# Performance work log

Measured on AMD Instinct MI355X. Metric: run time of the kernel, lower is better.

## Reference

```python
import jax, jax.numpy as jnp
import numpy as np

N_NODES = 100000
N_EDGES = 1600000


def setup_inputs() -> dict:
    key = jax.random.key(0)
    ks = jax.random.split(key, 8)
    x = jax.random.normal(ks[0], (N_NODES, 100), dtype=jnp.float32)
    edge_index = jax.random.randint(ks[1], (2, N_EDGES), 0, N_NODES, dtype=jnp.int64)
    edge_weight = jax.random.uniform(ks[2], (N_EDGES,), dtype=jnp.float32)
    # params (kaiming-ish scale)
    W_conv = jax.random.normal(ks[3], (100, 32), dtype=jnp.float32) * (1.0 / np.sqrt(100))
    b_conv = jnp.zeros((32,), jnp.float32)
    W1 = jax.random.normal(ks[4], (32, 16), dtype=jnp.float32) * (1.0 / np.sqrt(32))
    b1 = jnp.zeros((16,), jnp.float32)
    W2 = jax.random.normal(ks[5], (16, 8), dtype=jnp.float32) * (1.0 / np.sqrt(16))
    b2 = jnp.zeros((8,), jnp.float32)
    W3 = jax.random.normal(ks[6], (8, 10), dtype=jnp.float32) * (1.0 / np.sqrt(8))
    b3 = jnp.zeros((10,), jnp.float32)
    return {"x": x, "edge_index": edge_index, "edge_weight": edge_weight,
            "W_conv": W_conv, "b_conv": b_conv, "W1": W1, "b1": b1,
            "W2": W2, "b2": b2, "W3": W3, "b3": b3}


def gcn_conv(x, edge_index, W, b, n_nodes):
    # PyG GCNConv: add self-loops, symmetric deg^-0.5 normalization, unit edge weights
    loop = jnp.arange(n_nodes, dtype=edge_index.dtype)
    src = jnp.concatenate([edge_index[0], loop])
    dst = jnp.concatenate([edge_index[1], loop])
    deg = jax.ops.segment_sum(jnp.ones_like(dst, dtype=x.dtype), dst,
                              num_segments=n_nodes)
    dinv = jax.lax.rsqrt(jnp.maximum(deg, 1e-12))  # deg >= 1 due to self-loops
    norm = dinv[src] * dinv[dst]                   # [E+N]
    h = x @ W                                      # [N, 32]
    msg = h[src] * norm[:, None]                   # gather + scale
    out = jax.ops.segment_sum(msg, dst, num_segments=n_nodes)  # scatter-add
    return out + b


def reference(x, edge_index, edge_weight, W_conv, b_conv, W1, b1, W2, b2, W3, b3):
    # edge_weight is accepted by the original forward but never used (conv1(x, edge_index))
    n_nodes = x.shape[0]
    h = jax.nn.relu(gcn_conv(x, edge_index, W_conv, b_conv, n_nodes))
    # F.dropout with training=False (eval) is identity
    h = jax.nn.relu(h @ W1 + b1)
    h = jax.nn.relu(h @ W2 + b2)
    h = h @ W3 + b3
    return jax.nn.log_softmax(h, axis=1)
```

## Files before the change

kernel.cpp:

```cpp
#include <hip/hip_runtime.h>
#include <hip/hip_fp16.h>
#include <math.h>

#define N_NODES 100000
#define N_EDGES 1600000
#define F_IN 100
#define F_H 32

#define BKT_SHIFT 7
#define BKT_C 128
#define NBK 782
#define BKT_CAP 2560

#define BF_B 1024
#define BF_EPT 8
#define BF_TILE 8192
#define BF_GRID 196

#define XW_ROWS 256
#define XW_S2 51
#define XW_GRID 391

#define FUSE_GRID (BF_GRID + XW_GRID)
#define SM_BYTES 58624

#define AG_B 512
#define AG_CAP BKT_CAP
#define AG_EPT 5

__global__ __launch_bounds__(BF_B) void fused1_kernel(
        const int* __restrict__ src, const int* __restrict__ dst,
        int* __restrict__ gcursor, unsigned* __restrict__ packed,
        const float* __restrict__ x, const float* __restrict__ W,
        float* __restrict__ h2f) {
    __shared__ char smraw[SM_BYTES] __attribute__((aligned(16)));
    int t = threadIdx.x;
    if (blockIdx.x < BF_GRID) {
        int* cnt = (int*)smraw;
        int* lbase = cnt + NBK;
        int* gbase = lbase + NBK;
        int* wsums = gbase + NBK;
        int* ptot = wsums + 16;
        unsigned* stage = (unsigned*)(ptot + 1);
        unsigned short* stageB = (unsigned short*)(stage + BF_TILE);
        long base = (long)blockIdx.x * BF_TILE;
        for (int i = t; i < NBK; i += BF_B) cnt[i] = 0;
        __syncthreads();
        int myb[BF_EPT]; int mypos[BF_EPT]; unsigned mypk[BF_EPT];
#pragma unroll
        for (int k = 0; k < BF_EPT; k++) {
            long e = base + t + (long)k * BF_B;
            myb[k] = -1;
            if (e < N_EDGES) {
                int d = dst[e];
                int sI = src[e];
                int b = d >> BKT_SHIFT;
                myb[k] = b;
                mypk[k] = (unsigned)sI | ((unsigned)(d & (BKT_C - 1)) << 17);
                mypos[k] = atomicAdd(&cnt[b], 1);
            }
        }
        __syncthreads();
        if (t < NBK && cnt[t] > 0)
            gbase[t] = t * BKT_CAP + atomicAdd(&gcursor[t], cnt[t]);
        int lane = t & 63, w = t >> 6;
        int v = (t < NBK) ? cnt[t] : 0;
        int sc = v;
#pragma unroll
        for (int off = 1; off < 64; off <<= 1) {
            int xx = __shfl_up(sc, off, 64);
            if (lane >= off) sc += xx;
        }
        if (lane == 63) wsums[w] = sc;
        __syncthreads();
        int pre = 0;
#pragma unroll
        for (int u = 0; u < 16; u++) pre += (u < w) ? wsums[u] : 0;
        int incl = sc + pre;
        if (t < NBK) lbase[t] = incl - v;
        if (t == BF_B - 1) ptot[0] = incl;
        __syncthreads();
#pragma unroll
        for (int k = 0; k < BF_EPT; k++) {
            if (myb[k] >= 0) {
                int p = lbase[myb[k]] + mypos[k];
                stage[p] = mypk[k];
                stageB[p] = (unsigned short)myb[k];
            }
        }
        __syncthreads();
        int T = ptot[0];
        for (int i = t; i < T; i += BF_B) {
            int b = stageB[i];
            packed[gbase[b] + (i - lbase[b])] = stage[i];
        }
    } else {
        __half2* xs = (__half2*)smraw;
        int rbase = (blockIdx.x - BF_GRID) * XW_ROWS;
        int rows = min(XW_ROWS, N_NODES - rbase);
        int total = rows * F_IN;
        const float4* gx4 = (const float4*)(x + (long)rbase * F_IN);
        for (int i4 = t; i4 < (total >> 2); i4 += BF_B) {
            float4 v = gx4[i4];
            int i = i4 << 2;
            int r = i / F_IN;
            int k = i - r * F_IN;
            __half2* p = xs + r * XW_S2 + (k >> 1);
            p[0] = __floats2half2_rn(v.x, v.y);
            p[1] = __floats2half2_rn(v.z, v.w);
        }
        __syncthreads();
        int r = t & (XW_ROWS - 1);
        int colbase = __builtin_amdgcn_readfirstlane((t >> 8) << 3);
        if (r < rows) {
            const float* Wp = W + colbase;
            float acc[8];
#pragma unroll
            for (int j = 0; j < 8; j++) acc[j] = 0.f;
            const __half2* xr = xs + r * XW_S2;
#pragma unroll 5
            for (int k2 = 0; k2 < F_IN / 2; k2++) {
                float2 xv = __half22float2(xr[k2]);
#pragma unroll
                for (int j = 0; j < 8; j++)
                    acc[j] = fmaf(xv.y, Wp[(2 * k2 + 1) * F_H + j],
                                  fmaf(xv.x, Wp[(2 * k2) * F_H + j], acc[j]));
            }
            float4* dst4 = (float4*)(h2f + (long)(rbase + r) * F_H + colbase);
            dst4[0] = make_float4(acc[0], acc[1], acc[2], acc[3]);
            dst4[1] = make_float4(acc[4], acc[5], acc[6], acc[7]);
        }
    }
}

__global__ __launch_bounds__(256) void scale_kernel(
        const int* __restrict__ blen, const unsigned* __restrict__ packed,
        const float* __restrict__ h2f, __half* __restrict__ h2) {
    __shared__ int cnt[BKT_C];
    __shared__ float sdv[BKT_C];
    int t = threadIdx.x;
    int b = blockIdx.x;
    if (t < BKT_C) cnt[t] = 0;
    __syncthreads();
    int beg = b * BKT_CAP, end = beg + blen[b];
    for (int i = beg + t; i < end; i += 256)
        atomicAdd(&cnt[(packed[i] >> 17) & (BKT_C - 1)], 1);
    __syncthreads();
    if (t < BKT_C) sdv[t] = rsqrtf((float)cnt[t] + 1.0f);
    __syncthreads();
    int rbase = b << BKT_SHIFT;
    int rows = min(BKT_C, N_NODES - rbase);
    const float4* src4 = (const float4*)(h2f + (long)rbase * F_H);
    float2* dst2 = (float2*)h2;
    for (int i4 = t; i4 < rows * 8; i4 += 256) {
        float4 v = src4[i4];
        float dv = sdv[i4 >> 3];
        float2 o;
        __half2* oh = (__half2*)&o;
        oh[0] = __floats2half2_rn(v.x * dv, v.y * dv);
        oh[1] = __floats2half2_rn(v.z * dv, v.w * dv);
        dst2[(long)rbase * 8 + i4] = o;
    }
}

__global__ __launch_bounds__(AG_B) void agg_kernel(
        const int* __restrict__ blen, const unsigned* __restrict__ packed,
        const __half* __restrict__ h2,
        const float* __restrict__ bc,
        const float* __restrict__ W1, const float* __restrict__ b1,
        const float* __restrict__ W2, const float* __restrict__ b2,
        const float* __restrict__ W3, const float* __restrict__ b3,
        float* __restrict__ out) {
    __shared__ float accL[BKT_C * 33];
    __shared__ int esrc[AG_CAP];
    __shared__ int cnt[BKT_C];
    __shared__ int lbase[BKT_C];
    __shared__ int wsum;
    __shared__ float sbc[32], sW1[512], sb1[16], sW2[128], sb2[8], sW3[80], sb3[10];
    int t = threadIdx.x;
    if (t < 32) sbc[t] = bc[t];
    if (t < 512) sW1[t] = W1[t];
    if (t < 16) sb1[t] = b1[t];
    if (t < 128) sW2[t] = W2[t];
    if (t < 8) sb2[t] = b2[t];
    if (t < 80) sW3[t] = W3[t];
    if (t < 10) sb3[t] = b3[t];

    int b = blockIdx.x;
    int beg = b * BKT_CAP;
    int cnum = blen[b];
    if (t < BKT_C) cnt[t] = 0;
    __syncthreads();
    unsigned pk[AG_EPT]; int pos[AG_EPT];
#pragma unroll
    for (int k = 0; k < AG_EPT; k++) {
        int idx = t + k * AG_B;
        pk[k] = 0xFFFFFFFFu;
        if (idx < cnum) {
            unsigned p = packed[beg + idx];
            pk[k] = p;
            pos[k] = atomicAdd(&cnt[(p >> 17) & (BKT_C - 1)], 1);
        }
    }
    __syncthreads();
    {
        int lane = t & 63;
        int v = 0;
        if (t < BKT_C) {
            v = cnt[t];
#pragma unroll
            for (int off = 1; off < 64; off <<= 1) {
                int xx = __shfl_up(v, off, 64);
                if (lane >= off) v += xx;
            }
            if (t == 63) wsum = v;
        }
        __syncthreads();
        if (t < BKT_C) {
            if (t >= 64) v += wsum;
            lbase[t] = v;
        }
    }
    __syncthreads();
#pragma unroll
    for (int k = 0; k < AG_EPT; k++) {
        if (pk[k] != 0xFFFFFFFFu) {
            int lid = (pk[k] >> 17) & (BKT_C - 1);
            esrc[lbase[lid] - cnt[lid] + pos[k]] = (int)(pk[k] & 0x1FFFF);
        }
    }
    __syncthreads();
    {
        int g = t >> 2, l = t & 3;
        const float4* h2o = (const float4*)h2;
        int e = lbase[g] - cnt[g];
        int eend = lbase[g];
        float a0 = 0.f, a1 = 0.f, a2 = 0.f, a3 = 0.f;
        float a4 = 0.f, a5 = 0.f, a6 = 0.f, a7 = 0.f;
        for (; e + 8 <= eend; e += 8) {
            int s0 = esrc[e], s1 = esrc[e+1], s2 = esrc[e+2], s3 = esrc[e+3];
            int s4 = esrc[e+4], s5 = esrc[e+5], s6 = esrc[e+6], s7 = esrc[e+7];
            float4 q0 = h2o[s0 * 4 + l];
            float4 q1 = h2o[s1 * 4 + l];
            float4 q2 = h2o[s2 * 4 + l];
            float4 q3 = h2o[s3 * 4 + l];
            float4 q4 = h2o[s4 * 4 + l];
            float4 q5 = h2o[s5 * 4 + l];
            float4 q6 = h2o[s6 * 4 + l];
            float4 q7 = h2o[s7 * 4 + l];
#pragma unroll
            for (int u = 0; u < 8; u++) {
                float4 q = (u == 0) ? q0 : (u == 1) ? q1 : (u == 2) ? q2 :
                           (u == 3) ? q3 : (u == 4) ? q4 : (u == 5) ? q5 :
                           (u == 6) ? q6 : q7;
                const __half2* hp = (const __half2*)&q;
                float2 f0 = __half22float2(hp[0]);
                float2 f1 = __half22float2(hp[1]);
                float2 f2 = __half22float2(hp[2]);
                float2 f3 = __half22float2(hp[3]);
                a0 += f0.x; a1 += f0.y; a2 += f1.x; a3 += f1.y;
                a4 += f2.x; a5 += f2.y; a6 += f3.x; a7 += f3.y;
            }
        }
        for (; e < eend; e++) {
            float4 q = h2o[esrc[e] * 4 + l];
            const __half2* hp = (const __half2*)&q;
            float2 f0 = __half22float2(hp[0]);
            float2 f1 = __half22float2(hp[1]);
            float2 f2 = __half22float2(hp[2]);
            float2 f3 = __half22float2(hp[3]);
            a0 += f0.x; a1 += f0.y; a2 += f1.x; a3 += f1.y;
            a4 += f2.x; a5 += f2.y; a6 += f3.x; a7 += f3.y;
        }
        float* ap = accL + g * 33 + 8 * l;
        ap[0] = a0; ap[1] = a1; ap[2] = a2; ap[3] = a3;
        ap[4] = a4; ap[5] = a5; ap[6] = a6; ap[7] = a7;
    }
    __syncthreads();

    int n = (b << BKT_SHIFT) + t;
    if (t < BKT_C && n < N_NODES) {
        float dv = rsqrtf((float)cnt[t] + 1.0f);
        const __half2* h2v = (const __half2*)h2;
        float a[32];
#pragma unroll
        for (int q = 0; q < 16; q++) {
            float2 hv = __half22float2(h2v[n * 16 + q]);
            a[2*q]   = fmaxf((accL[t * 33 + 2*q]   + hv.x) * dv + sbc[2*q],   0.f);
            a[2*q+1] = fmaxf((accL[t * 33 + 2*q+1] + hv.y) * dv + sbc[2*q+1], 0.f);
        }
        float t1[16];
#pragma unroll
        for (int j = 0; j < 16; j++) {
            float s = sb1[j];
            for (int k = 0; k < 32; k++) s += a[k] * sW1[k * 16 + j];
            t1[j] = fmaxf(s, 0.f);
        }
        float t2[8];
#pragma unroll
        for (int j = 0; j < 8; j++) {
            float s = sb2[j];
            for (int k = 0; k < 16; k++) s += t1[k] * sW2[k * 8 + j];
            t2[j] = fmaxf(s, 0.f);
        }
        float t3[10];
#pragma unroll
        for (int j = 0; j < 10; j++) {
            float s = sb3[j];
            for (int k = 0; k < 8; k++) s += t2[k] * sW3[k * 10 + j];
            t3[j] = s;
        }
        float m = t3[0];
#pragma unroll
        for (int j = 1; j < 10; j++) m = fmaxf(m, t3[j]);
        float se = 0.f;
#pragma unroll
        for (int j = 0; j < 10; j++) se += expf(t3[j] - m);
        float lse = logf(se) + m;
        float* op = out + (long)n * 10;
#pragma unroll
        for (int j = 0; j < 10; j++) op[j] = t3[j] - lse;
    }
}

extern "C" void kernel_launch(void* const* d_in, const int* in_sizes, int n_in,
                              void* d_out, int out_size, void* d_ws, size_t ws_size,
                              hipStream_t stream) {
    const float* x  = (const float*)d_in[0];
    const int*   ei = (const int*)d_in[1];
    const float* Wc = (const float*)d_in[3];
    const float* bc = (const float*)d_in[4];
    const float* W1 = (const float*)d_in[5];
    const float* b1 = (const float*)d_in[6];
    const float* W2 = (const float*)d_in[7];
    const float* b2 = (const float*)d_in[8];
    const float* W3 = (const float*)d_in[9];
    const float* b3 = (const float*)d_in[10];
    float* out = (float*)d_out;

    __half*   h2      = (__half*)d_ws;
    unsigned* packed  = (unsigned*)((char*)d_ws + (long)N_NODES * F_H * 2);
    float*    h2f     = (float*)(packed + (long)NBK * BKT_CAP);
    int*      gcursor = (int*)(h2f + (long)N_NODES * F_H);

    const int* srcp = ei;
    const int* dstp = ei + N_EDGES;

    hipMemsetAsync(gcursor, 0, NBK * sizeof(int), stream);
    fused1_kernel<<<FUSE_GRID, BF_B, 0, stream>>>(srcp, dstp, gcursor, packed,
                                                  x, Wc, h2f);
    scale_kernel<<<NBK, 256, 0, stream>>>(gcursor, packed, h2f, h2);
    agg_kernel<<<NBK, AG_B, 0, stream>>>(gcursor, packed, h2, bc, W1, b1,
                                         W2, b2, W3, b3, out);
}
```

Before: 171.0 us.

## Fuse scale and aggregate kernels via cooperative grid sync; halve XW block count

```diff
diff --git a/kernel.cpp b/kernel.cpp
--- a/kernel.cpp
+++ b/kernel.cpp
@@ -1,6 +1,9 @@
 #include <hip/hip_runtime.h>
 #include <hip/hip_fp16.h>
+#include <hip/hip_cooperative_groups.h>
 #include <math.h>
+
+namespace cg = cooperative_groups;
 
 #define N_NODES 100000
 #define N_EDGES 1600000
@@ -19,9 +22,10 @@
 
 #define XW_ROWS 256
 #define XW_S2 51
-#define XW_GRID 391
-
-#define FUSE_GRID (BF_GRID + XW_GRID)
+#define XW_BLOCKS 196
+#define XW_TILES 2
+
+#define FUSE_GRID (BF_GRID + XW_BLOCKS)
 #define SM_BYTES 58624
 
 #define AG_B 512
@@ -96,40 +100,218 @@
         }
     } else {
         __half2* xs = (__half2*)smraw;
-        int rbase = (blockIdx.x - BF_GRID) * XW_ROWS;
-        int rows = min(XW_ROWS, N_NODES - rbase);
-        int total = rows * F_IN;
-        const float4* gx4 = (const float4*)(x + (long)rbase * F_IN);
-        for (int i4 = t; i4 < (total >> 2); i4 += BF_B) {
-            float4 v = gx4[i4];
-            int i = i4 << 2;
-            int r = i / F_IN;
-            int k = i - r * F_IN;
-            __half2* p = xs + r * XW_S2 + (k >> 1);
-            p[0] = __floats2half2_rn(v.x, v.y);
-            p[1] = __floats2half2_rn(v.z, v.w);
-        }
-        __syncthreads();
-        int r = t & (XW_ROWS - 1);
-        int colbase = __builtin_amdgcn_readfirstlane((t >> 8) << 3);
-        if (r < rows) {
-            const float* Wp = W + colbase;
-            float acc[8];
-#pragma unroll
-            for (int j = 0; j < 8; j++) acc[j] = 0.f;
-            const __half2* xr = xs + r * XW_S2;
+        for (int tile = 0; tile < XW_TILES; ++tile) {
+            int tb = (blockIdx.x - BF_GRID) * XW_TILES + tile;
+            int rbase = tb * XW_ROWS;
+            int rows = min(XW_ROWS, N_NODES - rbase);
+            if (rows <= 0) break;
+            if (tile) __syncthreads();
+            int total = rows * F_IN;
+            const float4* gx4 = (const float4*)(x + (long)rbase * F_IN);
+            for (int i4 = t; i4 < (total >> 2); i4 += BF_B) {
+                float4 v = gx4[i4];
+                int i = i4 << 2;
+                int r = i / F_IN;
+                int k = i - r * F_IN;
+                __half2* p = xs + r * XW_S2 + (k >> 1);
+                p[0] = __floats2half2_rn(v.x, v.y);
+                p[1] = __floats2half2_rn(v.z, v.w);
+            }
+            __syncthreads();
+            int r = t & (XW_ROWS - 1);
+            int colbase = __builtin_amdgcn_readfirstlane((t >> 8) << 3);
+            if (r < rows) {
+                const float* Wp = W + colbase;
+                float acc[8];
+#pragma unroll
+                for (int j = 0; j < 8; j++) acc[j] = 0.f;
+                const __half2* xr = xs + r * XW_S2;
 #pragma unroll 5
-            for (int k2 = 0; k2 < F_IN / 2; k2++) {
-                float2 xv = __half22float2(xr[k2]);
-#pragma unroll
-                for (int j = 0; j < 8; j++)
-                    acc[j] = fmaf(xv.y, Wp[(2 * k2 + 1) * F_H + j],
-                                  fmaf(xv.x, Wp[(2 * k2) * F_H + j], acc[j]));
-            }
-            float4* dst4 = (float4*)(h2f + (long)(rbase + r) * F_H + colbase);
-            dst4[0] = make_float4(acc[0], acc[1], acc[2], acc[3]);
-            dst4[1] = make_float4(acc[4], acc[5], acc[6], acc[7]);
-        }
+                for (int k2 = 0; k2 < F_IN / 2; k2++) {
+                    float2 xv = __half22float2(xr[k2]);
+#pragma unroll
+                    for (int j = 0; j < 8; j++)
+                        acc[j] = fmaf(xv.y, Wp[(2 * k2 + 1) * F_H + j],
+                                      fmaf(xv.x, Wp[(2 * k2) * F_H + j], acc[j]));
+                }
+                float4* dst4 = (float4*)(h2f + (long)(rbase + r) * F_H + colbase);
+                dst4[0] = make_float4(acc[0], acc[1], acc[2], acc[3]);
+                dst4[1] = make_float4(acc[4], acc[5], acc[6], acc[7]);
+            }
+        }
+    }
+}
+
+__global__ __launch_bounds__(AG_B, 8) void scagg_kernel(
+        const int* __restrict__ blen, const unsigned* __restrict__ packed,
+        const float* __restrict__ h2f, __half* __restrict__ h2,
+        const float* __restrict__ bc,
+        const float* __restrict__ W1, const float* __restrict__ b1,
+        const float* __restrict__ W2, const float* __restrict__ b2,
+        const float* __restrict__ W3, const float* __restrict__ b3,
+        float* __restrict__ out) {
+    __shared__ float accL[BKT_C * 33];
+    __shared__ int esrc[AG_CAP];
+    __shared__ int cnt[BKT_C];
+    __shared__ int lbase[BKT_C];
+    __shared__ float sdv[BKT_C];
+    __shared__ int wsum;
+    __shared__ float sbc[32], sW1[512], sb1[16], sW2[128], sb2[8], sW3[80], sb3[10];
+    int t = threadIdx.x;
+    if (t < 32) sbc[t] = bc[t];
+    if (t < 512) sW1[t] = W1[t];
+    if (t < 16) sb1[t] = b1[t];
+    if (t < 128) sW2[t] = W2[t];
+    if (t < 8) sb2[t] = b2[t];
+    if (t < 80) sW3[t] = W3[t];
+    if (t < 10) sb3[t] = b3[t];
+
+    int b = blockIdx.x;
+    int beg = b * BKT_CAP;
+    int cnum = blen[b];
+    if (t < BKT_C) cnt[t] = 0;
+    __syncthreads();
+    unsigned pk[AG_EPT]; int pos[AG_EPT];
+#pragma unroll
+    for (int k = 0; k < AG_EPT; k++) {
+        int idx = t + k * AG_B;
+        pk[k] = 0xFFFFFFFFu;
+        if (idx < cnum) {
+            unsigned p = packed[beg + idx];
+            pk[k] = p;
+            pos[k] = atomicAdd(&cnt[(p >> 17) & (BKT_C - 1)], 1);
+        }
+    }
+    __syncthreads();
+    {
+        int lane = t & 63;
+        int v = 0;
+        if (t < BKT_C) {
+            sdv[t] = rsqrtf((float)cnt[t] + 1.0f);
+            v = cnt[t];
+#pragma unroll
+            for (int off = 1; off < 64; off <<= 1) {
+                int xx = __shfl_up(v, off, 64);
+                if (lane >= off) v += xx;
+            }
+            if (t == 63) wsum = v;
+        }
+        __syncthreads();
+        if (t < BKT_C) {
+            if (t >= 64) v += wsum;
+            lbase[t] = v;
+        }
+    }
+    __syncthreads();
+    int rbase = b << BKT_SHIFT;
+    int rows = min(BKT_C, N_NODES - rbase);
+    {
+        const float4* s4 = (const float4*)(h2f + (long)rbase * F_H);
+        float2* d2 = (float2*)h2;
+        for (int i4 = t; i4 < rows * 8; i4 += AG_B) {
+            float4 vv = s4[i4];
+            float dv = sdv[i4 >> 3];
+            float2 o;
+            __half2* oh = (__half2*)&o;
+            oh[0] = __floats2half2_rn(vv.x * dv, vv.y * dv);
+            oh[1] = __floats2half2_rn(vv.z * dv, vv.w * dv);
+            d2[(long)rbase * 8 + i4] = o;
+        }
+    }
+#pragma unroll
+    for (int k = 0; k < AG_EPT; k++) {
+        if (pk[k] != 0xFFFFFFFFu) {
+            int lid = (pk[k] >> 17) & (BKT_C - 1);
+            esrc[lbase[lid] - cnt[lid] + pos[k]] = (int)(pk[k] & 0x1FFFF);
+        }
+    }
+    __threadfence();
+    cg::this_grid().sync();
+    __threadfence();
+
+    {
+        int g = t >> 2, l = t & 3;
+        const float4* h2o = (const float4*)h2;
+        int e = lbase[g] - cnt[g];
+        int eend = lbase[g];
+        float a0 = 0.f, a1 = 0.f, a2 = 0.f, a3 = 0.f;
+        float a4 = 0.f, a5 = 0.f, a6 = 0.f, a7 = 0.f;
+        for (; e + 4 <= eend; e += 4) {
+            int s0 = esrc[e], s1 = esrc[e+1], s2 = esrc[e+2], s3 = esrc[e+3];
+            float4 q0 = h2o[s0 * 4 + l];
+            float4 q1 = h2o[s1 * 4 + l];
+            float4 q2 = h2o[s2 * 4 + l];
+            float4 q3 = h2o[s3 * 4 + l];
+#pragma unroll
+            for (int u = 0; u < 4; u++) {
+                float4 q = (u == 0) ? q0 : (u == 1) ? q1 : (u == 2) ? q2 : q3;
+                const __half2* hp = (const __half2*)&q;
+                float2 f0 = __half22float2(hp[0]);
+                float2 f1 = __half22float2(hp[1]);
+                float2 f2 = __half22float2(hp[2]);
+                float2 f3 = __half22float2(hp[3]);
+                a0 += f0.x; a1 += f0.y; a2 += f1.x; a3 += f1.y;
+                a4 += f2.x; a5 += f2.y; a6 += f3.x; a7 += f3.y;
+            }
+        }
+        for (; e < eend; e++) {
+            float4 q = h2o[esrc[e] * 4 + l];
+            const __half2* hp = (const __half2*)&q;
+            float2 f0 = __half22float2(hp[0]);
+            float2 f1 = __half22float2(hp[1]);
+            float2 f2 = __half22float2(hp[2]);
+            float2 f3 = __half22float2(hp[3]);
+            a0 += f0.x; a1 += f0.y; a2 += f1.x; a3 += f1.y;
+            a4 += f2.x; a5 += f2.y; a6 += f3.x; a7 += f3.y;
+        }
+        float* ap = accL + g * 33 + 8 * l;
+        ap[0] = a0; ap[1] = a1; ap[2] = a2; ap[3] = a3;
+        ap[4] = a4; ap[5] = a5; ap[6] = a6; ap[7] = a7;
+    }
+    __syncthreads();
+
+    int n = (b << BKT_SHIFT) + t;
+    if (t < BKT_C && n < N_NODES) {
+        float dv = sdv[t];
+        const __half2* h2v = (const __half2*)h2;
+        float a[32];
+#pragma unroll
+        for (int q = 0; q < 16; q++) {
+            float2 hv = __half22float2(h2v[n * 16 + q]);
+            a[2*q]   = fmaxf((accL[t * 33 + 2*q]   + hv.x) * dv + sbc[2*q],   0.f);
+            a[2*q+1] = fmaxf((accL[t * 33 + 2*q+1] + hv.y) * dv + sbc[2*q+1], 0.f);
+        }
+        float t1[16];
+#pragma unroll
+        for (int j = 0; j < 16; j++) {
+            float s = sb1[j];
+            for (int k = 0; k < 32; k++) s += a[k] * sW1[k * 16 + j];
+            t1[j] = fmaxf(s, 0.f);
+        }
+        float t2[8];
+#pragma unroll
+        for (int j = 0; j < 8; j++) {
+            float s = sb2[j];
+            for (int k = 0; k < 16; k++) s += t1[k] * sW2[k * 8 + j];
+            t2[j] = fmaxf(s, 0.f);
+        }
+        float t3[10];
+#pragma unroll
+        for (int j = 0; j < 10; j++) {
+            float s = sb3[j];
+            for (int k = 0; k < 8; k++) s += t2[k] * sW3[k * 10 + j];
+            t3[j] = s;
+        }
+        float m = t3[0];
+#pragma unroll
+        for (int j = 1; j < 10; j++) m = fmaxf(m, t3[j]);
+        float se = 0.f;
+#pragma unroll
+        for (int j = 0; j < 10; j++) se += expf(t3[j] - m);
+        float lse = logf(se) + m;
+        float* op = out + (long)n * 10;
+#pragma unroll
+        for (int j = 0; j < 10; j++) op[j] = t3[j] - lse;
     }
 }
 
@@ -349,7 +531,23 @@
     hipMemsetAsync(gcursor, 0, NBK * sizeof(int), stream);
     fused1_kernel<<<FUSE_GRID, BF_B, 0, stream>>>(srcp, dstp, gcursor, packed,
                                                   x, Wc, h2f);
-    scale_kernel<<<NBK, 256, 0, stream>>>(gcursor, packed, h2f, h2);
-    agg_kernel<<<NBK, AG_B, 0, stream>>>(gcursor, packed, h2, bc, W1, b1,
-                                         W2, b2, W3, b3, out);
+
+    static int coop = -1;
+    if (coop < 0) {
+        int nb = 0;
+        hipError_t e = hipOccupancyMaxActiveBlocksPerMultiprocessor(
+                &nb, scagg_kernel, AG_B, 0);
+        coop = (e == hipSuccess && nb * 256 >= NBK) ? 1 : 0;
+    }
+    if (coop) {
+        void* kargs[] = {(void*)&gcursor, (void*)&packed, (void*)&h2f, (void*)&h2,
+                         (void*)&bc, (void*)&W1, (void*)&b1, (void*)&W2, (void*)&b2,
+                         (void*)&W3, (void*)&b3, (void*)&out};
+        hipLaunchCooperativeKernel(scagg_kernel, dim3(NBK), dim3(AG_B),
+                                   kargs, 0, stream);
+    } else {
+        scale_kernel<<<NBK, 256, 0, stream>>>(gcursor, packed, h2f, h2);
+        agg_kernel<<<NBK, AG_B, 0, stream>>>(gcursor, packed, h2, bc, W1, b1,
+                                             W2, b2, W3, b3, out);
+    }
 }
```

Result: slower. 174.8 us (+2.2%).
